# Kernel tuning notes

Hardware: AMD Instinct MI355X
Metric: run time of the kernel (lower is better)

## Reference

```python
import jax, jax.numpy as jnp
import numpy as np

B, L, S, DIM, NH = 4, 1024, 1024, 1024, 16
DH = DIM // NH


def setup_inputs() -> dict:
    key = jax.random.key(0)
    ks = jax.random.split(key, 16)
    std = 0.02
    inp = {
        'q': jax.random.normal(ks[0], (B, L, DIM), jnp.float32),
        'k': jax.random.normal(ks[1], (B, S, DIM), jnp.float32),
        'v': jax.random.normal(ks[2], (B, S, DIM), jnp.float32),
        'attn_mask': jax.random.bernoulli(ks[3], 0.9, (B, L, S)),
        'pos_bias': jax.random.normal(ks[4], (B, NH, L, S), jnp.float32),
        'Wq': jax.random.normal(ks[5], (DIM, DIM), jnp.float32) * std,
        'bq': jnp.zeros((DIM,), jnp.float32),
        'Wk': jax.random.normal(ks[6], (DIM, DIM), jnp.float32) * std,
        'bk': jnp.zeros((DIM,), jnp.float32),
        'Wv': jax.random.normal(ks[7], (DIM, DIM), jnp.float32) * std,
        'bv': jnp.zeros((DIM,), jnp.float32),
        'Wp': jax.random.normal(ks[8], (DIM, DIM), jnp.float32) * std,
        'bp': jnp.zeros((DIM,), jnp.float32),
        'is_causal': 1,
    }
    return inp


def _attention(q, k, v, attn_mask, pos_bias, Wq, bq, Wk, bk, Wv, bv, Wp, bp, is_causal):
    b, l, _ = q.shape
    s = k.shape[1]
    qh = (q @ Wq + bq).reshape(b, l, NH, DH)   # (B,L,nH,dh)
    kh = (k @ Wk + bk).reshape(b, s, NH, DH)
    vh = (v @ Wv + bv).reshape(b, s, NH, DH)

    mask = attn_mask  # (B,L,S) bool
    if is_causal:
        causal = jnp.tril(jnp.ones((l, l), dtype=bool))
        causal = jnp.pad(causal, ((0, 0), (s - l, 0)), constant_values=True)  # (L,S)
        mask = mask & causal[None]
    # rows with no allowed key attend everywhere (matches torch row-fix)
    row_any = mask.any(axis=-1, keepdims=True)
    mask = jnp.where(row_any, mask, True)

    bias = jnp.where(mask[:, None, :, :], pos_bias, -jnp.inf)  # (B,nH,L,S)
    scale = 1.0 / np.sqrt(DH).astype(np.float32)
    scores = jnp.einsum('blhd,bshd->bhls', qh, kh) * scale + bias
    attn = jax.nn.softmax(scores, axis=-1)
    o = jnp.einsum('bhls,bshd->blhd', attn, vh).reshape(b, l, NH * DH)
    return o @ Wp + bp


def reference(q, k, v, attn_mask, pos_bias, Wq, bq, Wk, bk, Wv, bv, Wp, bp, is_causal):
    return _attention(q, k, v, attn_mask, pos_bias, Wq, bq, Wk, bk, Wv, bv, Wp, bp, is_causal)
```

## Files before the change

kernel.cpp:

```cpp
#include <hip/hip_runtime.h>
#include <hip/hip_bf16.h>

typedef __hip_bfloat16 bf16;
typedef __attribute__((ext_vector_type(4))) float  floatx4;
typedef __attribute__((ext_vector_type(8))) short  short8;
typedef __attribute__((ext_vector_type(8))) __bf16 bf16x8;

constexpr int Bc = 4, Lc = 1024, Sc = 1024, DIMc = 1024, NHc = 16, DHc = 64;

template <typename V>
__device__ auto mfma_bf16_sel(V a, V b, floatx4 c, int)
    -> decltype(__builtin_amdgcn_mfma_f32_16x16x32_bf16(a, b, c, 0, 0, 0)) {
  return __builtin_amdgcn_mfma_f32_16x16x32_bf16(a, b, c, 0, 0, 0);
}
template <typename V>
__device__ floatx4 mfma_bf16_sel(V a, V b, floatx4 c, long) {
  bf16x8 a2 = __builtin_bit_cast(bf16x8, a);
  bf16x8 b2 = __builtin_bit_cast(bf16x8, b);
  return __builtin_amdgcn_mfma_f32_16x16x32_bf16(a2, b2, c, 0, 0, 0);
}
__device__ inline floatx4 mfma_bf16(short8 a, short8 b, floatx4 c) {
  return mfma_bf16_sel(a, b, c, 0);
}

union U8 { uint4 u; bf16 h[8]; };

__device__ inline U8 load8(const float* p) {
    float4 f0 = ((const float4*)p)[0];
    float4 f1 = ((const float4*)p)[1];
    U8 t;
    t.h[0] = __float2bfloat16(f0.x); t.h[1] = __float2bfloat16(f0.y);
    t.h[2] = __float2bfloat16(f0.z); t.h[3] = __float2bfloat16(f0.w);
    t.h[4] = __float2bfloat16(f1.x); t.h[5] = __float2bfloat16(f1.y);
    t.h[6] = __float2bfloat16(f1.z); t.h[7] = __float2bfloat16(f1.w);
    return t;
}

__global__ __launch_bounds__(256)
void prep_kernel(const float* __restrict__ Wq, const float* __restrict__ Wk,
                 const float* __restrict__ Wv, const float* __restrict__ Wp,
                 const int* __restrict__ mask, const int* __restrict__ is_causal_p,
                 bf16* __restrict__ wqt, bf16* __restrict__ wkt,
                 bf16* __restrict__ wvt, bf16* __restrict__ wpt,
                 unsigned long long* __restrict__ mbits,
                 int* __restrict__ rowany_g)
{
    __shared__ float tile[64][68];
    const int tid = threadIdx.x;
    int blk = blockIdx.x;

    if (blk < 1024) {
        const int w  = blk >> 8, t2 = blk & 255;
        const float* W  = (w == 0) ? Wq : (w == 1) ? Wk : (w == 2) ? Wv : Wp;
        bf16*        Wt = (w == 0) ? wqt : (w == 1) ? wkt : (w == 2) ? wvt : wpt;
        const int tk = (t2 >> 4) << 6;
        const int tn = (t2 & 15) << 6;
        #pragma unroll
        for (int i = 0; i < 4; ++i) {
            const int r = (tid >> 4) + i * 16;
            const int c = (tid & 15) << 2;
            *(float4*)(&tile[r][c]) =
                *(const float4*)(W + (size_t)(tk + r) * DIMc + tn + c);
        }
        __syncthreads();
        #pragma unroll
        for (int j = 0; j < 2; ++j) {
            const int nn = tid >> 2;
            const int kc = (tid & 3) + j * 4;
            U8 o;
            #pragma unroll
            for (int u = 0; u < 8; ++u)
                o.h[u] = __float2bfloat16(tile[kc * 8 + u][nn]);
            *(uint4*)(Wt + (size_t)(tn + nn) * DIMc + tk + kc * 8) = o.u;
        }
    } else {
        const int mb  = blk - 1024;
        const int rIb = tid >> 4;
        const int w   = tid & 15;
        const int row = mb * 16 + rIb;
        const int l   = row & (Lc - 1);
        const bool causal = (is_causal_p[0] != 0);

        const int4* mr4 = (const int4*)(mask + (size_t)row * Sc + w * 64);
        unsigned long long bits = 0ull;
        #pragma unroll
        for (int i = 0; i < 16; ++i) {
            int4 m4 = mr4[i];
            unsigned long long nib =
                (unsigned long long)((m4.x != 0) | ((m4.y != 0) << 1) |
                                     ((m4.z != 0) << 2) | ((m4.w != 0) << 3));
            bits |= nib << (4 * i);
        }
        mbits[(size_t)row * 16 + w] = bits;

        const int limit = causal ? l : (Sc - 1);
        const int base  = w * 64;
        unsigned long long am;
        if (limit >= base + 63)  am = bits;
        else if (limit < base)   am = 0ull;
        else                     am = bits & ((2ull << (limit - base)) - 1ull);
        unsigned long long red = am;
        #pragma unroll
        for (int d2 = 1; d2 < 16; d2 <<= 1) red |= __shfl_xor(red, d2);
        if (w == 0) rowany_g[row] = (red != 0ull) ? 1 : 0;
    }
}

constexpr int GPAD = 72;

__global__ __launch_bounds__(256)
void gemm_qkv_kernel(const float* __restrict__ q, const float* __restrict__ k,
                     const float* __restrict__ v,
                     const bf16* __restrict__ wqt, const bf16* __restrict__ wkt,
                     const bf16* __restrict__ wvt,
                     const float* __restrict__ bq, const float* __restrict__ bk,
                     const float* __restrict__ bv,
                     bf16* __restrict__ qh, bf16* __restrict__ kh,
                     bf16* __restrict__ vt)
{
    __shared__ bf16 As[128 * GPAD];
    __shared__ bf16 Bs[128 * GPAD];

    const int z = blockIdx.z;
    const float* A    = (z == 0) ? q   : (z == 1) ? k   : v;
    const bf16*  Bt   = (z == 0) ? wqt : (z == 1) ? wkt : wvt;
    const float* bias = (z == 0) ? bq  : (z == 1) ? bk  : bv;
    bf16*        out  = (z == 0) ? qh  : (z == 1) ? kh  : vt;

    const int tid  = threadIdx.x;
    const int wave = tid >> 6;
    const int lane = tid & 63;
    const int n = lane & 15, g = lane >> 4;
    const int m0 = blockIdx.x * 128;
    const int n0 = blockIdx.y * 128;
    const int wq_m = (wave & 1) * 64, wq_n = (wave >> 1) * 64;

    floatx4 acc[4][4];
    #pragma unroll
    for (int a = 0; a < 4; ++a)
        #pragma unroll
        for (int b2 = 0; b2 < 4; ++b2)
            acc[a][b2] = (floatx4){0.f, 0.f, 0.f, 0.f};

    const int srow   = tid >> 3;
    const int schunk = (tid & 7) * 8;

    for (int k0 = 0; k0 < DIMc; k0 += 64) {
        #pragma unroll
        for (int i = 0; i < 4; ++i) {
            const int r = srow + i * 32;
            U8 a8 = load8(A + (size_t)(m0 + r) * DIMc + k0 + schunk);
            *(uint4*)(&As[r * GPAD + schunk]) = a8.u;
            *(uint4*)(&Bs[r * GPAD + schunk]) =
                *(const uint4*)(Bt + (size_t)(n0 + r) * DIMc + k0 + schunk);
        }
        __syncthreads();
        #pragma unroll
        for (int ks = 0; ks < 2; ++ks) {
            short8 af[4], bf_[4];
            #pragma unroll
            for (int t = 0; t < 4; ++t) {
                af[t]  = *(const short8*)(&As[(wq_m + t * 16 + n) * GPAD + ks * 32 + g * 8]);
                bf_[t] = *(const short8*)(&Bs[(wq_n + t * 16 + n) * GPAD + ks * 32 + g * 8]);
            }
            #pragma unroll
            for (int tm = 0; tm < 4; ++tm)
                #pragma unroll
                for (int tn = 0; tn < 4; ++tn)
                    acc[tm][tn] = mfma_bf16(af[tm], bf_[tn], acc[tm][tn]);
        }
        __syncthreads();
    }

    #pragma unroll
    for (int tn = 0; tn < 4; ++tn) {
        const int col = n0 + wq_n + tn * 16 + n;
        const float bval = bias[col];
        #pragma unroll
        for (int tm = 0; tm < 4; ++tm) {
            #pragma unroll
            for (int r = 0; r < 4; ++r) {
                const int row = m0 + wq_m + tm * 16 + g * 4 + r;
                const float vv = acc[tm][tn][r] + bval;
                const int bb = row >> 10, ll = row & (Lc - 1);
                const int hh = col >> 6,  dd = col & 63;
                size_t idx;
                if (z < 2) idx = (((size_t)(bb * NHc + hh) * Lc + ll) * DHc) + dd;
                else       idx = (((size_t)(bb * NHc + hh) * DHc + dd) * Sc) + ll;
                out[idx] = __float2bfloat16(vv);
            }
        }
    }
}

__global__ __launch_bounds__(256)
void gemm_out_kernel(const bf16* __restrict__ A, const bf16* __restrict__ Bt,
                     const float* __restrict__ bias, float* __restrict__ out)
{
    __shared__ bf16 As[128 * GPAD];
    __shared__ bf16 Bs[128 * GPAD];

    const int tid  = threadIdx.x;
    const int wave = tid >> 6;
    const int lane = tid & 63;
    const int n = lane & 15, g = lane >> 4;
    const int m0 = blockIdx.x * 128;
    const int n0 = blockIdx.y * 128;
    const int wq_m = (wave & 1) * 64, wq_n = (wave >> 1) * 64;

    floatx4 acc[4][4];
    #pragma unroll
    for (int a = 0; a < 4; ++a)
        #pragma unroll
        for (int b2 = 0; b2 < 4; ++b2)
            acc[a][b2] = (floatx4){0.f, 0.f, 0.f, 0.f};

    const int srow   = tid >> 3;
    const int schunk = (tid & 7) * 8;

    for (int k0 = 0; k0 < DIMc; k0 += 64) {
        #pragma unroll
        for (int i = 0; i < 4; ++i) {
            const int r = srow + i * 32;
            *(uint4*)(&As[r * GPAD + schunk]) =
                *(const uint4*)(A + (size_t)(m0 + r) * DIMc + k0 + schunk);
            *(uint4*)(&Bs[r * GPAD + schunk]) =
                *(const uint4*)(Bt + (size_t)(n0 + r) * DIMc + k0 + schunk);
        }
        __syncthreads();
        #pragma unroll
        for (int ks = 0; ks < 2; ++ks) {
            short8 af[4], bf_[4];
            #pragma unroll
            for (int t = 0; t < 4; ++t) {
                af[t]  = *(const short8*)(&As[(wq_m + t * 16 + n) * GPAD + ks * 32 + g * 8]);
                bf_[t] = *(const short8*)(&Bs[(wq_n + t * 16 + n) * GPAD + ks * 32 + g * 8]);
            }
            #pragma unroll
            for (int tm = 0; tm < 4; ++tm)
                #pragma unroll
                for (int tn = 0; tn < 4; ++tn)
                    acc[tm][tn] = mfma_bf16(af[tm], bf_[tn], acc[tm][tn]);
        }
        __syncthreads();
    }

    #pragma unroll
    for (int tn = 0; tn < 4; ++tn) {
        const int col = n0 + wq_n + tn * 16 + n;
        const float bval = bias[col];
        #pragma unroll
        for (int tm = 0; tm < 4; ++tm) {
            #pragma unroll
            for (int r = 0; r < 4; ++r) {
                const int row = m0 + wq_m + tm * 16 + g * 4 + r;
                out[(size_t)row * DIMc + col] = acc[tm][tn][r] + bval;
            }
        }
    }
}

constexpr int PADk = 72;

__global__ __launch_bounds__(256)
void flash_attn_kernel(const bf16* __restrict__ qh, const bf16* __restrict__ kh,
                       const bf16* __restrict__ vt,
                       const unsigned long long* __restrict__ mbits,
                       const int* __restrict__ rowany_g,
                       const float* __restrict__ pos_bias,
                       const int* __restrict__ is_causal_p, bf16* __restrict__ o)
{
    __shared__ bf16 Ks[64 * PADk];
    __shared__ bf16 Vs[64 * PADk];
    __shared__ bf16 Pw[4][16 * PADk];
    __shared__ int rowany[64];
    __shared__ int hasfix_s;

    const int tid  = threadIdx.x;
    const int lane = tid & 63;
    const int wave = tid >> 6;
    const int n = lane & 15;
    const int g = lane >> 4;

    const int qt = blockIdx.x & 15;
    const int bh = blockIdx.x >> 4;
    const int h  = bh & (NHc - 1);
    const int b  = bh >> 4;
    const int l0 = qt * 64;
    const bool causal = (is_causal_p[0] != 0);

    if (tid == 0) hasfix_s = 0;
    __syncthreads();
    if (tid < 64) {
        const int ra = rowany_g[(b << 10) + l0 + tid];
        rowany[tid] = ra;
        if (ra == 0) atomicOr(&hasfix_s, 1);
    }
    __syncthreads();
    const bool hasfix = (hasfix_s != 0);

    const int qrow_frag = l0 + wave * 16 + n;
    const bf16* qp = qh + ((size_t)bh * Lc + qrow_frag) * DHc;
    const short8 qf0 = *(const short8*)(qp + g * 8);
    const short8 qf1 = *(const short8*)(qp + 32 + g * 8);

    floatx4 oacc[4];
    #pragma unroll
    for (int t = 0; t < 4; ++t) oacc[t] = (floatx4){0.f, 0.f, 0.f, 0.f};
    float m_run[4], l_run[4];
    #pragma unroll
    for (int r = 0; r < 4; ++r) { m_run[r] = -3.0e38f; l_run[r] = 0.f; }

    int nchunk = Sc / 64;
    if (causal && !hasfix) nchunk = qt + 1;

    for (int c = 0; c < nchunk; ++c) {
        const int s0 = c * 64;
        __syncthreads();
        #pragma unroll
        for (int it = 0; it < 2; ++it) {
            const int e  = tid * 8 + it * 2048;
            const int r0 = e >> 6, c0 = e & 63;
            *(uint4*)(Ks + r0 * PADk + c0) =
                *(const uint4*)(kh + ((size_t)bh * Sc + s0 + r0) * DHc + c0);
            *(uint4*)(Vs + r0 * PADk + c0) =
                *(const uint4*)(vt + ((size_t)bh * DHc + r0) * Sc + s0 + c0);
        }
        __syncthreads();

        float bvv[4][4]; int nib[4];
        #pragma unroll
        for (int r = 0; r < 4; ++r) {
            const int l = l0 + wave * 16 + g * 4 + r;
            const float4 b4 =
                *(const float4*)(pos_bias + ((size_t)bh * Lc + l) * Sc + s0 + 4 * n);
            bvv[r][0] = b4.x; bvv[r][1] = b4.y; bvv[r][2] = b4.z; bvv[r][3] = b4.w;
            const unsigned long long wbits = mbits[((size_t)(b << 10) + l) * 16 + c];
            nib[r] = (int)((wbits >> (4 * n)) & 15ull);
        }

        floatx4 scv[4];
        #pragma unroll
        for (int t = 0; t < 4; ++t) scv[t] = (floatx4){0.f, 0.f, 0.f, 0.f};
        #pragma unroll
        for (int t = 0; t < 4; ++t) {
            const bf16* kp = Ks + (4 * n + t) * PADk + g * 8;
            short8 kb0 = *(const short8*)(kp);
            short8 kb1 = *(const short8*)(kp + 32);
            scv[t] = mfma_bf16(qf0, kb0, scv[t]);
            scv[t] = mfma_bf16(qf1, kb1, scv[t]);
        }

        #pragma unroll
        for (int r = 0; r < 4; ++r) {
            const int row = wave * 16 + g * 4 + r;
            const int l = l0 + row;
            const int limit = causal ? l : (Sc - 1);
            const bool fix = (rowany[row] == 0);
            float vals[4];
            #pragma unroll
            for (int t = 0; t < 4; ++t) {
                const int s = s0 + 4 * n + t;
                const bool ok = fix || (s <= limit && ((nib[r] >> t) & 1));
                vals[t] = ok ? scv[t][r] * 0.125f + bvv[r][t] : -3.0e38f;
            }
            float cm = fmaxf(fmaxf(vals[0], vals[1]), fmaxf(vals[2], vals[3]));
            cm = fmaxf(cm, __shfl_xor(cm, 1));
            cm = fmaxf(cm, __shfl_xor(cm, 2));
            cm = fmaxf(cm, __shfl_xor(cm, 4));
            cm = fmaxf(cm, __shfl_xor(cm, 8));
            const float mnew = fmaxf(m_run[r], cm);
            const float alpha = __expf(m_run[r] - mnew);
            float csum = 0.f;
            union PK { uint2 u; bf16 hb[4]; } pk;
            #pragma unroll
            for (int t = 0; t < 4; ++t) {
                const float p = (vals[t] < -1.0e37f) ? 0.f : __expf(vals[t] - mnew);
                csum += p;
                pk.hb[t] = __float2bfloat16(p);
            }
            *(uint2*)(&Pw[wave][(row & 15) * PADk + 4 * n]) = pk.u;
            csum += __shfl_xor(csum, 1);
            csum += __shfl_xor(csum, 2);
            csum += __shfl_xor(csum, 4);
            csum += __shfl_xor(csum, 8);
            l_run[r] = l_run[r] * alpha + csum;
            m_run[r] = mnew;
            #pragma unroll
            for (int t = 0; t < 4; ++t) oacc[t][r] *= alpha;
        }

        #pragma unroll
        for (int sc2 = 0; sc2 < 2; ++sc2) {
            short8 pa = *(const short8*)(Pw[wave] + n * PADk + sc2 * 32 + g * 8);
            #pragma unroll
            for (int t = 0; t < 4; ++t) {
                short8 vb = *(const short8*)(Vs + (16 * t + n) * PADk + sc2 * 32 + g * 8);
                oacc[t] = mfma_bf16(pa, vb, oacc[t]);
            }
        }
    }

    #pragma unroll
    for (int r = 0; r < 4; ++r) {
        const int l = l0 + wave * 16 + g * 4 + r;
        const float inv = 1.f / l_run[r];
        #pragma unroll
        for (int t = 0; t < 4; ++t) {
            const int d = 16 * t + n;
            o[((size_t)(b * Lc + l)) * DIMc + h * DHc + d] =
                __float2bfloat16(oacc[t][r] * inv);
        }
    }
}

extern "C" void kernel_launch(void* const* d_in, const int* in_sizes, int n_in,
                              void* d_out, int out_size, void* d_ws, size_t ws_size,
                              hipStream_t stream)
{
    (void)in_sizes; (void)n_in; (void)out_size; (void)ws_size;

    const float* q        = (const float*)d_in[0];
    const float* k        = (const float*)d_in[1];
    const float* v        = (const float*)d_in[2];
    const int*   mask     = (const int*)d_in[3];
    const float* pos_bias = (const float*)d_in[4];
    const float* Wq = (const float*)d_in[5];
    const float* bq = (const float*)d_in[6];
    const float* Wk = (const float*)d_in[7];
    const float* bk = (const float*)d_in[8];
    const float* Wv = (const float*)d_in[9];
    const float* bv = (const float*)d_in[10];
    const float* Wp = (const float*)d_in[11];
    const float* bp = (const float*)d_in[12];
    const int*   is_causal = (const int*)d_in[13];

    const size_t per = (size_t)Bc * NHc * Lc * DHc;
    const size_t wsz = (size_t)DIMc * DIMc;
    bf16* qh  = (bf16*)d_ws;
    bf16* kh  = qh + per;
    bf16* vt  = kh + per;
    bf16* oh  = vt + per;
    bf16* wqt = oh + per;
    bf16* wkt = wqt + wsz;
    bf16* wvt = wkt + wsz;
    bf16* wpt = wvt + wsz;
    unsigned long long* mbits = (unsigned long long*)(wpt + wsz);
    int* rowany_g = (int*)(mbits + (size_t)Bc * Lc * 16);
    float* outp = (float*)d_out;

    dim3 bb(256);

    prep_kernel<<<1280, bb, 0, stream>>>(Wq, Wk, Wv, Wp, mask, is_causal,
                                         wqt, wkt, wvt, wpt, mbits, rowany_g);

    dim3 gq(32, 8, 3);
    gemm_qkv_kernel<<<gq, bb, 0, stream>>>(q, k, v, wqt, wkt, wvt,
                                           bq, bk, bv, qh, kh, vt);

    flash_attn_kernel<<<(Bc * NHc) * (Lc / 64), bb, 0, stream>>>(
        qh, kh, vt, mbits, rowany_g, pos_bias, is_causal, oh);

    dim3 gg(32, 8);
    gemm_out_kernel<<<gg, bb, 0, stream>>>(oh, wpt, bp, outp);
}
```

Before: 589.5 us.

## Register-prefetch next tiles in GEMMs and attention, reorder attention blocks heavy-first

```diff
diff --git a/kernel.cpp b/kernel.cpp
--- a/kernel.cpp
+++ b/kernel.cpp
@@ -25,9 +25,7 @@
 
 union U8 { uint4 u; bf16 h[8]; };
 
-__device__ inline U8 load8(const float* p) {
-    float4 f0 = ((const float4*)p)[0];
-    float4 f1 = ((const float4*)p)[1];
+__device__ inline U8 cvt8(float4 f0, float4 f1) {
     U8 t;
     t.h[0] = __float2bfloat16(f0.x); t.h[1] = __float2bfloat16(f0.y);
     t.h[2] = __float2bfloat16(f0.z); t.h[3] = __float2bfloat16(f0.w);
@@ -145,16 +143,36 @@
     const int srow   = tid >> 3;
     const int schunk = (tid & 7) * 8;
 
+    float4 a0[4], a1[4]; uint4 bR[4];
+    #pragma unroll
+    for (int i = 0; i < 4; ++i) {
+        const float* ap = A + (size_t)(m0 + srow + i * 32) * DIMc + schunk;
+        a0[i] = ((const float4*)ap)[0];
+        a1[i] = ((const float4*)ap)[1];
+        bR[i] = *(const uint4*)(Bt + (size_t)(n0 + srow + i * 32) * DIMc + schunk);
+    }
+
     for (int k0 = 0; k0 < DIMc; k0 += 64) {
+        __syncthreads();
         #pragma unroll
         for (int i = 0; i < 4; ++i) {
             const int r = srow + i * 32;
-            U8 a8 = load8(A + (size_t)(m0 + r) * DIMc + k0 + schunk);
-            *(uint4*)(&As[r * GPAD + schunk]) = a8.u;
-            *(uint4*)(&Bs[r * GPAD + schunk]) =
-                *(const uint4*)(Bt + (size_t)(n0 + r) * DIMc + k0 + schunk);
-        }
-        __syncthreads();
+            U8 t = cvt8(a0[i], a1[i]);
+            *(uint4*)(&As[r * GPAD + schunk]) = t.u;
+            *(uint4*)(&Bs[r * GPAD + schunk]) = bR[i];
+        }
+        __syncthreads();
+        if (k0 + 64 < DIMc) {
+            #pragma unroll
+            for (int i = 0; i < 4; ++i) {
+                const float* ap =
+                    A + (size_t)(m0 + srow + i * 32) * DIMc + k0 + 64 + schunk;
+                a0[i] = ((const float4*)ap)[0];
+                a1[i] = ((const float4*)ap)[1];
+                bR[i] = *(const uint4*)(Bt + (size_t)(n0 + srow + i * 32) * DIMc +
+                                        k0 + 64 + schunk);
+            }
+        }
         #pragma unroll
         for (int ks = 0; ks < 2; ++ks) {
             short8 af[4], bf_[4];
@@ -169,7 +187,6 @@
                 for (int tn = 0; tn < 4; ++tn)
                     acc[tm][tn] = mfma_bf16(af[tm], bf_[tn], acc[tm][tn]);
         }
-        __syncthreads();
     }
 
     #pragma unroll
@@ -218,16 +235,31 @@
     const int srow   = tid >> 3;
     const int schunk = (tid & 7) * 8;
 
+    uint4 aR[4], bR[4];
+    #pragma unroll
+    for (int i = 0; i < 4; ++i) {
+        aR[i] = *(const uint4*)(A  + (size_t)(m0 + srow + i * 32) * DIMc + schunk);
+        bR[i] = *(const uint4*)(Bt + (size_t)(n0 + srow + i * 32) * DIMc + schunk);
+    }
+
     for (int k0 = 0; k0 < DIMc; k0 += 64) {
+        __syncthreads();
         #pragma unroll
         for (int i = 0; i < 4; ++i) {
             const int r = srow + i * 32;
-            *(uint4*)(&As[r * GPAD + schunk]) =
-                *(const uint4*)(A + (size_t)(m0 + r) * DIMc + k0 + schunk);
-            *(uint4*)(&Bs[r * GPAD + schunk]) =
-                *(const uint4*)(Bt + (size_t)(n0 + r) * DIMc + k0 + schunk);
-        }
-        __syncthreads();
+            *(uint4*)(&As[r * GPAD + schunk]) = aR[i];
+            *(uint4*)(&Bs[r * GPAD + schunk]) = bR[i];
+        }
+        __syncthreads();
+        if (k0 + 64 < DIMc) {
+            #pragma unroll
+            for (int i = 0; i < 4; ++i) {
+                aR[i] = *(const uint4*)(A  + (size_t)(m0 + srow + i * 32) * DIMc +
+                                        k0 + 64 + schunk);
+                bR[i] = *(const uint4*)(Bt + (size_t)(n0 + srow + i * 32) * DIMc +
+                                        k0 + 64 + schunk);
+            }
+        }
         #pragma unroll
         for (int ks = 0; ks < 2; ++ks) {
             short8 af[4], bf_[4];
@@ -242,7 +274,6 @@
                 for (int tn = 0; tn < 4; ++tn)
                     acc[tm][tn] = mfma_bf16(af[tm], bf_[tn], acc[tm][tn]);
         }
-        __syncthreads();
     }
 
     #pragma unroll
@@ -282,8 +313,8 @@
     const int n = lane & 15;
     const int g = lane >> 4;
 
-    const int qt = blockIdx.x & 15;
-    const int bh = blockIdx.x >> 4;
+    const int qt = 15 - (blockIdx.x >> 6);
+    const int bh = blockIdx.x & 63;
     const int h  = bh & (NHc - 1);
     const int b  = bh >> 4;
     const int l0 = qt * 64;
@@ -304,6 +335,31 @@
     const short8 qf0 = *(const short8*)(qp + g * 8);
     const short8 qf1 = *(const short8*)(qp + 32 + g * 8);
 
+    const int e0 = tid * 8,        r0a = e0 >> 6, c0a = e0 & 63;
+    const int e1 = tid * 8 + 2048, r0b = e1 >> 6, c0b = e1 & 63;
+    const bf16* kb0p = kh + ((size_t)bh * Sc + r0a) * DHc + c0a;
+    const bf16* kb1p = kh + ((size_t)bh * Sc + r0b) * DHc + c0b;
+    const bf16* vb0p = vt + ((size_t)bh * DHc + r0a) * Sc + c0a;
+    const bf16* vb1p = vt + ((size_t)bh * DHc + r0b) * Sc + c0b;
+    bf16* ksw0 = Ks + r0a * PADk + c0a;
+    bf16* ksw1 = Ks + r0b * PADk + c0b;
+    bf16* vsw0 = Vs + r0a * PADk + c0a;
+    bf16* vsw1 = Vs + r0b * PADk + c0b;
+
+    union F4 { float4 v; float f[4]; };
+    const float* brow[4];
+    const unsigned long long* mrow[4];
+    int limit_r[4]; bool fix_r[4];
+    #pragma unroll
+    for (int r = 0; r < 4; ++r) {
+        const int row = wave * 16 + g * 4 + r;
+        const int l = l0 + row;
+        brow[r] = pos_bias + ((size_t)bh * Lc + l) * Sc + 4 * n;
+        mrow[r] = mbits + ((size_t)(b << 10) + l) * 16;
+        limit_r[r] = causal ? l : (Sc - 1);
+        fix_r[r] = (rowany[row] == 0);
+    }
+
     floatx4 oacc[4];
     #pragma unroll
     for (int t = 0; t < 4; ++t) oacc[t] = (floatx4){0.f, 0.f, 0.f, 0.f};
@@ -314,30 +370,39 @@
     int nchunk = Sc / 64;
     if (causal && !hasfix) nchunk = qt + 1;
 
+    uint4 kr0 = *(const uint4*)(kb0p);
+    uint4 kr1 = *(const uint4*)(kb1p);
+    uint4 vr0 = *(const uint4*)(vb0p);
+    uint4 vr1 = *(const uint4*)(vb1p);
+    F4 bcur[4], bnxt[4];
+    unsigned long long mcur[4], mnxt[4];
+    #pragma unroll
+    for (int r = 0; r < 4; ++r) {
+        bcur[r].v = *(const float4*)(brow[r]);
+        mcur[r]   = mrow[r][0];
+    }
+
     for (int c = 0; c < nchunk; ++c) {
+        __syncthreads();
+        *(uint4*)ksw0 = kr0;  *(uint4*)ksw1 = kr1;
+        *(uint4*)vsw0 = vr0;  *(uint4*)vsw1 = vr1;
+        __syncthreads();
+
+        if (c + 1 < nchunk) {
+            const size_t ko = (size_t)(c + 1) * 4096;
+            const int    vo = (c + 1) * 64;
+            kr0 = *(const uint4*)(kb0p + ko);
+            kr1 = *(const uint4*)(kb1p + ko);
+            vr0 = *(const uint4*)(vb0p + vo);
+            vr1 = *(const uint4*)(vb1p + vo);
+            #pragma unroll
+            for (int r = 0; r < 4; ++r) {
+                bnxt[r].v = *(const float4*)(brow[r] + vo);
+                mnxt[r]   = mrow[r][c + 1];
+            }
+        }
+
         const int s0 = c * 64;
-        __syncthreads();
-        #pragma unroll
-        for (int it = 0; it < 2; ++it) {
-            const int e  = tid * 8 + it * 2048;
-            const int r0 = e >> 6, c0 = e & 63;
-            *(uint4*)(Ks + r0 * PADk + c0) =
-                *(const uint4*)(kh + ((size_t)bh * Sc + s0 + r0) * DHc + c0);
-            *(uint4*)(Vs + r0 * PADk + c0) =
-                *(const uint4*)(vt + ((size_t)bh * DHc + r0) * Sc + s0 + c0);
-        }
-        __syncthreads();
-
-        float bvv[4][4]; int nib[4];
-        #pragma unroll
-        for (int r = 0; r < 4; ++r) {
-            const int l = l0 + wave * 16 + g * 4 + r;
-            const float4 b4 =
-                *(const float4*)(pos_bias + ((size_t)bh * Lc + l) * Sc + s0 + 4 * n);
-            bvv[r][0] = b4.x; bvv[r][1] = b4.y; bvv[r][2] = b4.z; bvv[r][3] = b4.w;
-            const unsigned long long wbits = mbits[((size_t)(b << 10) + l) * 16 + c];
-            nib[r] = (int)((wbits >> (4 * n)) & 15ull);
-        }
 
         floatx4 scv[4];
         #pragma unroll
@@ -354,15 +419,13 @@
         #pragma unroll
         for (int r = 0; r < 4; ++r) {
             const int row = wave * 16 + g * 4 + r;
-            const int l = l0 + row;
-            const int limit = causal ? l : (Sc - 1);
-            const bool fix = (rowany[row] == 0);
+            const int nib = (int)((mcur[r] >> (4 * n)) & 15ull);
             float vals[4];
             #pragma unroll
             for (int t = 0; t < 4; ++t) {
                 const int s = s0 + 4 * n + t;
-                const bool ok = fix || (s <= limit && ((nib[r] >> t) & 1));
-                vals[t] = ok ? scv[t][r] * 0.125f + bvv[r][t] : -3.0e38f;
+                const bool ok = fix_r[r] || (s <= limit_r[r] && ((nib >> t) & 1));
+                vals[t] = ok ? scv[t][r] * 0.125f + bcur[r].f[t] : -3.0e38f;
             }
             float cm = fmaxf(fmaxf(vals[0], vals[1]), fmaxf(vals[2], vals[3]));
             cm = fmaxf(cm, __shfl_xor(cm, 1));
@@ -399,6 +462,9 @@
                 oacc[t] = mfma_bf16(pa, vb, oacc[t]);
             }
         }
+
+        #pragma unroll
+        for (int r = 0; r < 4; ++r) { bcur[r] = bnxt[r]; mcur[r] = mnxt[r]; }
     }
 
     #pragma unroll
```

After: 601.7 us. +2.1%, slower.
